# Optimization experiments

Measured on AMD Instinct MI355X. Metric: run time of the kernel, lower is better.

Reference implementation:

```python
import jax, jax.numpy as jnp
import numpy as np

NH = 10
EPS = 1e-10

def setup_inputs() -> dict:
    key = jax.random.key(0)
    k1, k2, k3, k4, k5 = jax.random.split(key, 5)
    b, n_s, e, n_t = 8, 8192, 32, 8192
    return {
        "x": jax.random.normal(k1, (b, n_s, e), dtype=jnp.float32),
        "rel_lon": jax.random.normal(k2, (n_t, n_s), dtype=jnp.float32),
        "rel_lat": jax.random.normal(k3, (n_t, n_s), dtype=jnp.float32),
        "coords_source": jax.random.uniform(k4, (n_s, 2), dtype=jnp.float32),
        "coords_target": jax.random.uniform(k5, (n_t, 2), dtype=jnp.float32),
    }

def reference(x, rel_lon, rel_lat, coords_source, coords_target):
    # ---- nn_layer: k-NN over precomputed relative coordinate matrices ----
    d_rel = jnp.sqrt(rel_lon ** 2 + rel_lat ** 2)          # [n_t, n_s]
    neg_d, idx = jax.lax.top_k(-d_rel, NH)                 # nh smallest distances
    indices_dist = -neg_d                                  # [n_t, nh]
    x_nearest = x[:, idx]                                  # [b, n_t, nh, e] gather
    indices_lon = jnp.take_along_axis(rel_lon, idx, axis=1)  # [n_t, nh]
    indices_lat = jnp.take_along_axis(rel_lat, idx, axis=1)  # [n_t, nh]
    # ---- interpolator: inverse-distance-weighted interpolation ----
    # pairwise target-source distances via the expanded form (avoids [n_t,n_s,2])
    t2 = jnp.sum(coords_target ** 2, axis=1)[:, None]      # [n_t, 1]
    s2 = jnp.sum(coords_source ** 2, axis=1)[None, :]      # [1, n_s]
    d2 = t2 + s2 - 2.0 * coords_target @ coords_source.T   # [n_t, n_s]
    d_ts = jnp.sqrt(jnp.maximum(d2, 1e-12))
    w = 1.0 / (d_ts + EPS)
    w = w / jnp.sum(w, axis=1, keepdims=True)              # [n_t, n_s]
    x_inter = jnp.einsum('bse,ts->bte', x, w)              # [b, n_t, e]
    return (x_nearest, x_inter, indices_dist, indices_lon, indices_lat)
```

## Files before the change

kernel.cpp:

```cpp
#include <hip/hip_runtime.h>
#include <hip/hip_bf16.h>
#include <stdint.h>

#define B_   8
#define NS_  8192
#define E_   32
#define NT_  8192
#define NH_  10
#define NCH_ 128
#define SCAP 128

typedef __bf16 bf16x8 __attribute__((ext_vector_type(8)));
typedef float  f32x4  __attribute__((ext_vector_type(4)));
typedef unsigned short ushort8_t __attribute__((ext_vector_type(8)));
typedef unsigned short ushort4_t __attribute__((ext_vector_type(4)));

static __device__ inline unsigned short f2bf(float f) {
  __hip_bfloat16 h = __float2bfloat16(f);
  return *reinterpret_cast<unsigned short*>(&h);
}
static __device__ inline float bf2f(unsigned short u) {
  __hip_bfloat16 h;
  *reinterpret_cast<unsigned short*>(&h) = u;
  return __bfloat162float(h);
}

static __device__ inline float tenth_smallest(float v, int lane) {
  unsigned long long kv =
      ((unsigned long long)__float_as_uint(v) << 32) | (unsigned)lane;
  float out = 0.f;
#pragma unroll
  for (int k = 0; k < NH_; ++k) {
    unsigned long long m = kv;
#pragma unroll
    for (int off = 32; off > 0; off >>= 1) {
      const unsigned long long o = __shfl_xor(m, off, 64);
      m = o < m ? o : m;
    }
    if (kv == m) kv = ~0ull;
    if (k == NH_ - 1) out = __uint_as_float((unsigned)(m >> 32));
  }
  return out;
}

union __align__(16) SharedU {
  struct {
    unsigned short Xl[8][256][8];
    unsigned short Rl[2][8][16][8];
    float RsumP[16][32];
    float RsumInv[32];
  } xi;
  struct {
    int cnt[8];
    unsigned int cand[8][SCAP];
  } tk;
};

__global__ __launch_bounds__(512) void mega_kernel(
    const float* __restrict__ rel_lon, const float* __restrict__ rel_lat,
    float* __restrict__ out_d, float* __restrict__ out_lon,
    float* __restrict__ out_lat, int* __restrict__ idx_out,
    const unsigned short* __restrict__ XT2, const float* __restrict__ cs,
    const float* __restrict__ ct, float* __restrict__ out_xi)
{
#pragma clang fp contract(off)
  __shared__ SharedU sh;
  const int tid = threadIdx.x;

  if (blockIdx.x < 256) {
    const int w = tid >> 6, l = tid & 63;
    const int mg = w >> 1, ng = w & 1;
    const int lcol = l & 15, lkg = l >> 4;
    const int t0 = blockIdx.x * 32;

    const int gt = tid & 31;
    const int gq = tid >> 5;
    const int gng = gt >> 4, glc = gt & 15;
    const int gk = gq >> 1;
    const int gsl = (gq & 1) * 4;
    const float2 ctg = ((const float2*)ct)[t0 + gt];
    const float t2g = ctg.x * ctg.x + ctg.y * ctg.y;
    float rpart = 0.f;

    const int t = t0 + ng * 16 + lcol;

    f32x4 acc[4];
#pragma unroll
    for (int m = 0; m < 4; ++m)
#pragma unroll
      for (int j = 0; j < 4; ++j) acc[m][j] = 0.f;

    for (int c = 0; c < NCH_; ++c) {
      {
        const unsigned short* gsrc =
            XT2 + ((size_t)c * 8 + w) * 2048 + (size_t)l * 8;
#pragma unroll
        for (int bg = 0; bg < 4; ++bg) {
          __builtin_amdgcn_global_load_lds(
              (const __attribute__((address_space(1))) void*)(gsrc + bg * 512),
              (__attribute__((address_space(3))) void*)&sh.xi.Xl[w][bg * 64][0],
              16, 0, 0);
        }
      }
      {
        const int sb = c * 64 + gq * 4;
        const float4 cA = *(const float4*)&cs[2 * sb];
        const float4 cB = *(const float4*)&cs[2 * sb + 4];
        const float sxv[4] = {cA.x, cA.z, cB.x, cB.z};
        const float syv[4] = {cA.y, cA.w, cB.y, cB.w};
        ushort4_t ro;
#pragma unroll
        for (int j = 0; j < 4; ++j) {
          const float sx = sxv[j], sy = syv[j];
          const float s2 = sx * sx + sy * sy;
          const float p0 = ctg.x * sx;
          const float dot = fmaf(ctg.y, sy, p0);
          const float ts = t2g + s2;
          float d2 = ts - 2.0f * dot;
          d2 = fmaxf(d2, 1e-12f);
          const float r = __builtin_amdgcn_rsqf(d2);
          const unsigned short ub = f2bf(r);
          ro[j] = ub;
          rpart += bf2f(ub);
        }
        *(ushort4_t*)&sh.xi.Rl[gng][gk][glc][gsl] = ro;
      }
      asm volatile("s_waitcnt vmcnt(0) lgkmcnt(0)" ::: "memory");
      __builtin_amdgcn_s_barrier();

#pragma unroll
      for (int half = 0; half < 2; ++half) {
        const bf16x8 Bf = *(const bf16x8*)&sh.xi.Rl[ng][half * 4 + lkg][lcol][0];
#pragma unroll
        for (int m = 0; m < 4; ++m) {
          const bf16x8 a = *(const bf16x8*)
              &sh.xi.Xl[half * 4 + lkg][(mg * 4 + m) * 16 + lcol][0];
          acc[m] =
              __builtin_amdgcn_mfma_f32_16x16x32_bf16(a, Bf, acc[m], 0, 0, 0);
        }
      }
      __builtin_amdgcn_s_barrier();
    }

    sh.xi.RsumP[gq][gt] = rpart;
    asm volatile("s_waitcnt lgkmcnt(0)" ::: "memory");
    __builtin_amdgcn_s_barrier();
    if (tid < 32) {
      float ssum = 0.f;
#pragma unroll
      for (int qq = 0; qq < 16; ++qq) ssum += sh.xi.RsumP[qq][tid];
      sh.xi.RsumInv[tid] = 1.0f / ssum;
    }
    asm volatile("s_waitcnt lgkmcnt(0)" ::: "memory");
    __builtin_amdgcn_s_barrier();
    const float ri = sh.xi.RsumInv[ng * 16 + lcol];

#pragma unroll
    for (int m = 0; m < 4; ++m) {
      const int be0 = (mg * 4 + m) * 16 + lkg * 4;
      const int b = be0 >> 5, e = be0 & 31;
      float4 o;
      o.x = acc[m][0] * ri;
      o.y = acc[m][1] * ri;
      o.z = acc[m][2] * ri;
      o.w = acc[m][3] * ri;
      *(float4*)&out_xi[((size_t)b * NT_ + t) * E_ + e] = o;
    }
  } else {
    const int q = tid >> 6;
    const int lane = tid & 63;
    const int t = blockIdx.x - 256;
    const float* lon_row = rel_lon + (size_t)t * NS_;
    const float* lat_row = rel_lat + (size_t)t * NS_;
    const int base = q * 1024;
    const float4* lon4 = (const float4*)(lon_row + base);
    const float4* lat4 = (const float4*)(lat_row + base);

    if (lane == 0) sh.tk.cnt[q] = 0;

    float d2v[4][4];
    float lmin = __uint_as_float(0x7f800000u);
#pragma unroll
    for (int p = 0; p < 4; ++p) {
      const float4 lo = lon4[p * 64 + lane];
      const float4 la = lat4[p * 64 + lane];
      d2v[p][0] = __fmaf_rn(lo.x, lo.x, __fmul_rn(la.x, la.x));
      d2v[p][1] = __fmaf_rn(lo.y, lo.y, __fmul_rn(la.y, la.y));
      d2v[p][2] = __fmaf_rn(lo.z, lo.z, __fmul_rn(la.z, la.z));
      d2v[p][3] = __fmaf_rn(lo.w, lo.w, __fmul_rn(la.w, la.w));
      lmin = fminf(lmin, fminf(fminf(d2v[p][0], d2v[p][1]),
                               fminf(d2v[p][2], d2v[p][3])));
    }
    const float T = tenth_smallest(lmin, lane) * 1.000002f;

#pragma unroll
    for (int p = 0; p < 4; ++p) {
      const float mn = fminf(fminf(d2v[p][0], d2v[p][1]),
                             fminf(d2v[p][2], d2v[p][3]));
      if (mn <= T) {
        const int s = base + p * 256 + lane * 4;
#pragma unroll
        for (int j = 0; j < 4; ++j) {
          if (d2v[p][j] <= T) {
            const int pos = atomicAdd(&sh.tk.cnt[q], 1);
            if (pos < SCAP) sh.tk.cand[q][pos] = (unsigned)(s + j);
          }
        }
      }
    }

    __syncthreads();

    if (q == 0) {
      unsigned long long top[NH_];
#pragma unroll
      for (int i = 0; i < NH_; ++i) top[i] = ~0ull;

#pragma unroll
      for (int seg = 0; seg < 8; ++seg) {
        const int nc = min(sh.tk.cnt[seg], SCAP);
#pragma unroll
        for (int cc = 0; cc < SCAP / 64; ++cc) {
          const int ci = lane + cc * 64;
          if (ci < nc) {
            const unsigned s = sh.tk.cand[seg][ci];
            const float lo = lon_row[s];
            const float la = lat_row[s];
            const float d = __fsqrt_rn(__fadd_rn(__fmul_rn(lo, lo),
                                                 __fmul_rn(la, la)));
            unsigned long long p =
                ((unsigned long long)__float_as_uint(d) << 32) | s;
#pragma unroll
            for (int i = 0; i < NH_; ++i) {
              const bool lt = p < top[i];
              const unsigned long long mn2 = lt ? p : top[i];
              const unsigned long long mx2 = lt ? top[i] : p;
              top[i] = mn2;
              p = mx2;
            }
          }
        }
      }

      unsigned long long resv = ~0ull;
      unsigned long long cur = top[0];
#pragma unroll
      for (int k = 0; k < NH_; ++k) {
        unsigned long long m = cur;
#pragma unroll
        for (int off = 32; off > 0; off >>= 1) {
          const unsigned long long o = __shfl_xor(m, off, 64);
          m = o < m ? o : m;
        }
        if (cur == m) {
#pragma unroll
          for (int i = 0; i < NH_ - 1; ++i) top[i] = top[i + 1];
          top[NH_ - 1] = ~0ull;
          cur = top[0];
        }
        if (lane == k) resv = m;
      }

      if (lane < NH_) {
        const unsigned s = (unsigned)(resv & 0xffffffffu);
        const float d = __uint_as_float((unsigned)(resv >> 32));
        out_d[t * NH_ + lane] = d;
        idx_out[t * NH_ + lane] = (int)s;
        out_lon[t * NH_ + lane] = lon_row[s];
        out_lat[t * NH_ + lane] = lat_row[s];
      }
    }
  }
}

__global__ __launch_bounds__(256) void gather_kernel(
    const float* __restrict__ x, const int* __restrict__ idxbuf,
    float* __restrict__ out_xn)
{
  const int t = blockIdx.x;
  __shared__ int sidx[NH_];
  if (threadIdx.x < NH_) sidx[threadIdx.x] = idxbuf[t * NH_ + threadIdx.x];
  __syncthreads();
  for (int i = threadIdx.x; i < B_ * NH_ * (E_ / 4); i += 256) {
    const int e4 = i & 7;
    const int k = (i >> 3) % NH_;
    const int b = (i >> 3) / NH_;
    const int s = sidx[k];
    const float4 v = *(const float4*)(x + ((size_t)b * NS_ + s) * E_ + e4 * 4);
    *(float4*)(out_xn + (((size_t)b * NT_ + t) * NH_ + k) * E_ + e4 * 4) = v;
  }
}

__global__ __launch_bounds__(256) void xprep_kernel(
    const float* __restrict__ x, unsigned short* __restrict__ XT2)
{
  __shared__ __align__(16) unsigned short T[32][136];
  const int b = blockIdx.y;
  const int s0 = blockIdx.x * 128;
  const int tid = threadIdx.x;
  const int eq = tid & 7, slq = tid >> 3;
#pragma unroll
  for (int r4 = 0; r4 < 4; ++r4) {
    const int sl = r4 * 32 + slq;
    const float4 v = *(const float4*)&x[((size_t)b * NS_ + s0 + sl) * E_ + eq * 4];
    T[eq * 4 + 0][sl] = f2bf(v.x);
    T[eq * 4 + 1][sl] = f2bf(v.y);
    T[eq * 4 + 2][sl] = f2bf(v.z);
    T[eq * 4 + 3][sl] = f2bf(v.w);
  }
  __syncthreads();
  const int r = tid & 31, cq = tid >> 5;
  const int be = b * 32 + r;
  const int sA = s0 + cq * 16;
  const int c = sA >> 6;
  const int kA = (sA >> 3) & 7;
  unsigned short* dst = XT2 + ((size_t)(c * 8 + kA) * 256 + be) * 8;
  *(ushort8_t*)dst = *(const ushort8_t*)&T[r][cq * 16];
  *(ushort8_t*)(dst + 2048) = *(const ushort8_t*)&T[r][cq * 16 + 8];
}

extern "C" void kernel_launch(void* const* d_in, const int* in_sizes, int n_in,
                              void* d_out, int out_size, void* d_ws,
                              size_t ws_size, hipStream_t stream)
{
  const float* x       = (const float*)d_in[0];
  const float* rel_lon = (const float*)d_in[1];
  const float* rel_lat = (const float*)d_in[2];
  const float* cs      = (const float*)d_in[3];
  const float* ct      = (const float*)d_in[4];

  float* out = (float*)d_out;
  float* out_xn  = out;
  float* out_xi  = out + (size_t)B_ * NT_ * NH_ * E_;
  float* out_d   = out_xi + (size_t)B_ * NT_ * E_;
  float* out_lon = out_d + (size_t)NT_ * NH_;
  float* out_lat = out_lon + (size_t)NT_ * NH_;

  int* idxbuf = (int*)d_ws;
  unsigned short* XT2 = (unsigned short*)out_xn;

  xprep_kernel<<<dim3(NS_ / 128, B_), 256, 0, stream>>>(x, XT2);
  mega_kernel<<<256 + NT_, 512, 0, stream>>>(rel_lon, rel_lat, out_d, out_lon,
                                             out_lat, idxbuf, XT2, cs, ct,
                                             out_xi);
  gather_kernel<<<NT_, 256, 0, stream>>>(x, idxbuf, out_xn);
}
```

Before: 253.5 us.

## Double-buffer X staging with half-size source chunks and raise wave priority

The interpolation loop now walks source chunks of 32 instead of 64 and double-buffers the X tile in LDS. The next chunk's async global-to-LDS load is issued before the current chunk's weights are computed, and only the older loads are waited on. The goal is to overlap global memory latency with weight computation and MFMA work. The blocks doing the interpolation also get a higher wave priority. In exchange the loop runs twice as many iterations, so it pays twice as many barriers, and the per-thread weight computation is narrower.

```diff
diff --git a/kernel.cpp b/kernel.cpp
--- a/kernel.cpp
+++ b/kernel.cpp
@@ -7,13 +7,13 @@
 #define E_   32
 #define NT_  8192
 #define NH_  10
-#define NCH_ 128
+#define NSC_ 256
 #define SCAP 128
 
 typedef __bf16 bf16x8 __attribute__((ext_vector_type(8)));
 typedef float  f32x4  __attribute__((ext_vector_type(4)));
 typedef unsigned short ushort8_t __attribute__((ext_vector_type(8)));
-typedef unsigned short ushort4_t __attribute__((ext_vector_type(4)));
+typedef unsigned short ushort2_t __attribute__((ext_vector_type(2)));
 
 static __device__ inline unsigned short f2bf(float f) {
   __hip_bfloat16 h = __float2bfloat16(f);
@@ -45,8 +45,8 @@
 
 union __align__(16) SharedU {
   struct {
-    unsigned short Xl[8][256][8];
-    unsigned short Rl[2][8][16][8];
+    unsigned short Xl[2][4][256][8];
+    unsigned short Rl[2][4][16][8];
     float RsumP[16][32];
     float RsumInv[32];
   } xi;
@@ -68,6 +68,8 @@
   const int tid = threadIdx.x;
 
   if (blockIdx.x < 256) {
+    __builtin_amdgcn_s_setprio(1);
+
     const int w = tid >> 6, l = tid & 63;
     const int mg = w >> 1, ng = w & 1;
     const int lcol = l & 15, lkg = l >> 4;
@@ -76,8 +78,8 @@
     const int gt = tid & 31;
     const int gq = tid >> 5;
     const int gng = gt >> 4, glc = gt & 15;
-    const int gk = gq >> 1;
-    const int gsl = (gq & 1) * 4;
+    const int gk = gq >> 2;
+    const int gsl = (gq & 3) * 2;
     const float2 ctg = ((const float2*)ct)[t0 + gt];
     const float t2g = ctg.x * ctg.x + ctg.y * ctg.y;
     float rpart = 0.f;
@@ -90,28 +92,35 @@
 #pragma unroll
       for (int j = 0; j < 4; ++j) acc[m][j] = 0.f;
 
-    for (int c = 0; c < NCH_; ++c) {
+#define STAGE_SC(buf, sc)                                                    \
+    {                                                                        \
+      const unsigned short* gbase =                                          \
+          XT2 + ((size_t)(((sc) >> 1) * 8 + ((sc)&1) * 4 + (w >> 1))) * 2048 \
+              + (w & 1) * 1024 + (size_t)l * 8;                              \
+      __builtin_amdgcn_global_load_lds(                                      \
+          (const __attribute__((address_space(1))) void*)gbase,              \
+          (__attribute__((address_space(3))) void*)                          \
+              &sh.xi.Xl[buf][w >> 1][(w & 1) * 128][0], 16, 0, 0);           \
+      __builtin_amdgcn_global_load_lds(                                      \
+          (const __attribute__((address_space(1))) void*)(gbase + 512),      \
+          (__attribute__((address_space(3))) void*)                          \
+              &sh.xi.Xl[buf][w >> 1][(w & 1) * 128 + 64][0], 16, 0, 0);      \
+    }
+
+    STAGE_SC(0, 0)
+    int cur = 0;
+    for (int sc = 0; sc < NSC_; ++sc) {
+      const bool more = (sc + 1 < NSC_);
+      if (more) STAGE_SC(cur ^ 1, sc + 1)
+
       {
-        const unsigned short* gsrc =
-            XT2 + ((size_t)c * 8 + w) * 2048 + (size_t)l * 8;
-#pragma unroll
-        for (int bg = 0; bg < 4; ++bg) {
-          __builtin_amdgcn_global_load_lds(
-              (const __attribute__((address_space(1))) void*)(gsrc + bg * 512),
-              (__attribute__((address_space(3))) void*)&sh.xi.Xl[w][bg * 64][0],
-              16, 0, 0);
-        }
-      }
-      {
-        const int sb = c * 64 + gq * 4;
+        const int sb = sc * 32 + gq * 2;
         const float4 cA = *(const float4*)&cs[2 * sb];
-        const float4 cB = *(const float4*)&cs[2 * sb + 4];
-        const float sxv[4] = {cA.x, cA.z, cB.x, cB.z};
-        const float syv[4] = {cA.y, cA.w, cB.y, cB.w};
-        ushort4_t ro;
-#pragma unroll
-        for (int j = 0; j < 4; ++j) {
-          const float sx = sxv[j], sy = syv[j];
+        ushort2_t ro;
+#pragma unroll
+        for (int j = 0; j < 2; ++j) {
+          const float sx = (j == 0) ? cA.x : cA.z;
+          const float sy = (j == 0) ? cA.y : cA.w;
           const float s2 = sx * sx + sy * sy;
           const float p0 = ctg.x * sx;
           const float dot = fmaf(ctg.y, sy, p0);
@@ -123,24 +132,25 @@
           ro[j] = ub;
           rpart += bf2f(ub);
         }
-        *(ushort4_t*)&sh.xi.Rl[gng][gk][glc][gsl] = ro;
-      }
-      asm volatile("s_waitcnt vmcnt(0) lgkmcnt(0)" ::: "memory");
+        *(ushort2_t*)&sh.xi.Rl[gng][gk][glc][gsl] = ro;
+      }
+      if (more)
+        asm volatile("s_waitcnt vmcnt(2) lgkmcnt(0)" ::: "memory");
+      else
+        asm volatile("s_waitcnt vmcnt(0) lgkmcnt(0)" ::: "memory");
       __builtin_amdgcn_s_barrier();
 
 #pragma unroll
-      for (int half = 0; half < 2; ++half) {
-        const bf16x8 Bf = *(const bf16x8*)&sh.xi.Rl[ng][half * 4 + lkg][lcol][0];
-#pragma unroll
-        for (int m = 0; m < 4; ++m) {
-          const bf16x8 a = *(const bf16x8*)
-              &sh.xi.Xl[half * 4 + lkg][(mg * 4 + m) * 16 + lcol][0];
-          acc[m] =
-              __builtin_amdgcn_mfma_f32_16x16x32_bf16(a, Bf, acc[m], 0, 0, 0);
-        }
+      for (int m = 0; m < 4; ++m) {
+        const bf16x8 a =
+            *(const bf16x8*)&sh.xi.Xl[cur][lkg][(mg * 4 + m) * 16 + lcol][0];
+        const bf16x8 Bf = *(const bf16x8*)&sh.xi.Rl[ng][lkg][lcol][0];
+        acc[m] = __builtin_amdgcn_mfma_f32_16x16x32_bf16(a, Bf, acc[m], 0, 0, 0);
       }
       __builtin_amdgcn_s_barrier();
-    }
+      cur ^= 1;
+    }
+#undef STAGE_SC
 
     sh.xi.RsumP[gq][gt] = rpart;
     asm volatile("s_waitcnt lgkmcnt(0)" ::: "memory");
```

New measurement: 271.2 us. 7.0% more time.
